# Kernel optimization log

Hardware: AMD Instinct MI355X
Metric: run time of the kernel (lower is better)

## Reference

```python
import jax, jax.numpy as jnp
import numpy as np
import math

B = 262144
N = 1000
BIAS = 0.5


def setup_inputs() -> dict:
    key = jax.random.key(0)
    kx, kk = jax.random.split(key)
    x = jax.random.uniform(kx, (B, 1), dtype=jnp.float32)
    K = jnp.asarray(10.0, dtype=jnp.float32)  # learned scalar parameter
    return {"x": x, "K": K}


def reference(x, K):
    # range_array = [1..N], range_diag scales column n by 1/n
    rng = jnp.arange(1, N + 1, dtype=jnp.float32)          # [N]
    xb = x + BIAS                                          # [B,1]
    # outer product: [B,1] @ [1,N] -> [B,N]
    s = jnp.sin((2.0 * math.pi / K) * (xb * rng[None, :])) # [B,N]
    # multiply by diag(1/n) then sum over columns == weighted sum
    out = jnp.sum(s / rng[None, :], axis=1)                # [B]
    out = out * (-K / math.pi) + (K / 2.0 - BIAS)
    return out
```

## Files before the change

kernel.cpp:

```cpp
#include <hip/hip_runtime.h>


constexpr int   NTERMS = 1000;
constexpr float BIASF  = 0.5f;
constexpr int   BLOCK  = 256;

__global__ __launch_bounds__(BLOCK)
void sawtooth_closed_kernel(const float* __restrict__ x,
                            const float* __restrict__ Kp,
                            float* __restrict__ out,
                            int nelem)
{
    const float K      = Kp[0];
    const float c      = 6.283185307179586f / K;
    const float scale  = -K * 0.3183098861837907f;
    const float offset = 0.5f * K - BIASF;
    const float M      = (float)(NTERMS + 1);
    const float invM   = 1.0f / M;
    const float invMM1 = 1.0f / (M * (M + 1.0f));

    const int base = (blockIdx.x * BLOCK + threadIdx.x) * 4;
    if (base + 3 >= nelem) return;

    const float4 xv = *reinterpret_cast<const float4*>(x + base);
    float4 r;

    #pragma unroll
    for (int j = 0; j < 4; ++j) {
        const float xj = (j == 0) ? xv.x : (j == 1) ? xv.y : (j == 2) ? xv.z : xv.w;
        const float th = c * (xj + BIASF);

        float sz, cz;  sincosf(th, &sz, &cz);
        float sp, cp;  sincosf(M * th, &sp, &cp);

        const float wi = sz / (2.0f - 2.0f * cz);

        const float Ar = 0.5f * cp - sp * wi;
        const float Ai = cp * wi + 0.5f * sp;
        const float zwr = 0.5f * cz - sz * wi;
        const float zwi = cz * wi + 0.5f * sz;

        const float ImT = Ai * invM - (Ar * zwi + Ai * zwr) * invMM1;

        const float partial = 0.5f * (3.14159265358979f - th) - ImT;
        const float o = fmaf(partial, scale, offset);
        if (j == 0) r.x = o; else if (j == 1) r.y = o; else if (j == 2) r.z = o; else r.w = o;
    }

    *reinterpret_cast<float4*>(out + base) = r;
}

extern "C" void kernel_launch(void* const* d_in, const int* in_sizes, int n_in,
                              void* d_out, int out_size, void* d_ws, size_t ws_size,
                              hipStream_t stream)
{
    const float* x  = (const float*)d_in[0];
    const float* Kp = (const float*)d_in[1];
    float* out      = (float*)d_out;

    const int nelem   = out_size;
    const int threads = (nelem + 3) / 4;
    const int grid    = (threads + BLOCK - 1) / BLOCK;

    sawtooth_closed_kernel<<<grid, BLOCK, 0, stream>>>(x, Kp, out, nelem);
}
```

Measured before the change: 10.93 us.

## Use hardware sin/cos in revolutions and simplify output to x plus tail

Replaces libm sincosf with the AMD hardware sin/cos intrinsics, which take their argument in revolutions. The large M*theta argument is range-reduced with floor, and the division becomes rcp. The sawtooth main term cancels algebraically, so the output is computed as x plus a scaled tail correction. It also switches from four elements per thread with float4 accesses to one element per thread. Hardware sin accuracy and cancellation could affect precision, and the scalar loads may cost some memory efficiency.

```diff
diff --git a/kernel.cpp b/kernel.cpp
--- a/kernel.cpp
+++ b/kernel.cpp
@@ -6,48 +6,42 @@
 constexpr int   BLOCK  = 256;
 
 __global__ __launch_bounds__(BLOCK)
-void sawtooth_closed_kernel(const float* __restrict__ x,
-                            const float* __restrict__ Kp,
-                            float* __restrict__ out,
-                            int nelem)
+void sawtooth_tail_kernel(const float* __restrict__ x,
+                          const float* __restrict__ Kp,
+                          float* __restrict__ out,
+                          int nelem)
 {
+    const int gid = blockIdx.x * BLOCK + threadIdx.x;
+    if (gid >= nelem) return;
+
     const float K      = Kp[0];
-    const float c      = 6.283185307179586f / K;
-    const float scale  = -K * 0.3183098861837907f;
-    const float offset = 0.5f * K - BIASF;
-    const float M      = (float)(NTERMS + 1);
-    const float invM   = 1.0f / M;
-    const float invMM1 = 1.0f / (M * (M + 1.0f));
+    const float invK   = __builtin_amdgcn_rcpf(K);
+    const float Kopi   = K * 0.3183098861837907f;
+    const float Mf     = (float)(NTERMS + 1);
+    const float invM   = 1.0f / Mf;
+    const float invMM1 = 1.0f / (Mf * (Mf + 1.0f));
 
-    const int base = (blockIdx.x * BLOCK + threadIdx.x) * 4;
-    if (base + 3 >= nelem) return;
+    const float xv = x[gid];
+    const float t  = (xv + BIASF) * invK;
 
-    const float4 xv = *reinterpret_cast<const float4*>(x + base);
-    float4 r;
+    const float sz = __builtin_amdgcn_sinf(t);
+    const float cz = __builtin_amdgcn_cosf(t);
 
-    #pragma unroll
-    for (int j = 0; j < 4; ++j) {
-        const float xj = (j == 0) ? xv.x : (j == 1) ? xv.y : (j == 2) ? xv.z : xv.w;
-        const float th = c * (xj + BIASF);
+    float u = t * Mf;
+    u -= __builtin_floorf(u);
+    const float sp = __builtin_amdgcn_sinf(u);
+    const float cp = __builtin_amdgcn_cosf(u);
 
-        float sz, cz;  sincosf(th, &sz, &cz);
-        float sp, cp;  sincosf(M * th, &sp, &cp);
+    const float wi = sz * __builtin_amdgcn_rcpf(2.0f - 2.0f * cz);
 
-        const float wi = sz / (2.0f - 2.0f * cz);
+    const float Ar  = fmaf(-sp, wi, 0.5f * cp);
+    const float Ai  = fmaf( cp, wi, 0.5f * sp);
+    const float zwr = fmaf(-sz, wi, 0.5f * cz);
+    const float zwi = fmaf( cz, wi, 0.5f * sz);
 
-        const float Ar = 0.5f * cp - sp * wi;
-        const float Ai = cp * wi + 0.5f * sp;
-        const float zwr = 0.5f * cz - sz * wi;
-        const float zwi = cz * wi + 0.5f * sz;
+    const float ImT = fmaf(-(Ar * zwi + Ai * zwr), invMM1, Ai * invM);
 
-        const float ImT = Ai * invM - (Ar * zwi + Ai * zwr) * invMM1;
-
-        const float partial = 0.5f * (3.14159265358979f - th) - ImT;
-        const float o = fmaf(partial, scale, offset);
-        if (j == 0) r.x = o; else if (j == 1) r.y = o; else if (j == 2) r.z = o; else r.w = o;
-    }
-
-    *reinterpret_cast<float4*>(out + base) = r;
+    out[gid] = fmaf(Kopi, ImT, xv);
 }
 
 extern "C" void kernel_launch(void* const* d_in, const int* in_sizes, int n_in,
@@ -58,9 +52,8 @@
     const float* Kp = (const float*)d_in[1];
     float* out      = (float*)d_out;
 
-    const int nelem   = out_size;
-    const int threads = (nelem + 3) / 4;
-    const int grid    = (threads + BLOCK - 1) / BLOCK;
+    const int nelem = out_size;
+    const int grid  = (nelem + BLOCK - 1) / BLOCK;
 
-    sawtooth_closed_kernel<<<grid, BLOCK, 0, stream>>>(x, Kp, out, nelem);
+    sawtooth_tail_kernel<<<grid, BLOCK, 0, stream>>>(x, Kp, out, nelem);
 }
```

Measured after the change: 9.931 us. -9.2%, faster.
